# Kernel tuning notes

Measured on AMD Instinct MI355X. Metric: run time of the kernel, lower is better.

Reference implementation:

```python
import jax, jax.numpy as jnp
from jax import lax
import numpy as np

K = 2000      # self.k: entries kept per sample
T_SC = 3      # number of IHT iterations
DN = ('NCHW', 'OIHW', 'NCHW')


def keep_k_largest(X, k):
    # Per-sample hard threshold: keep the k largest-magnitude entries of the
    # flattened [C,H,W] activations, zero the rest (exactly k kept, as in argsort).
    B = X.shape[0]
    flat = X.reshape(B, -1)                                # [B, N]
    _, idx = lax.top_k(jnp.abs(flat), k)                   # [B, k]
    vals = jnp.take_along_axis(flat, idx, axis=1)          # [B, k]
    out = jnp.zeros_like(flat).at[jnp.arange(B)[:, None], idx].set(vals)
    return out.reshape(X.shape)


def _D_apply(X, W_D):
    # ConvTranspose2d(numb_atom -> dp_channels), stride 1, no padding:
    # full correlation with the spatially flipped, io-swapped kernel.
    kh, kw = W_D.shape[2], W_D.shape[3]
    Wt = jnp.flip(jnp.transpose(W_D, (1, 0, 2, 3)), (2, 3))  # [dp, atoms, kh, kw]
    return lax.conv_general_dilated(X, Wt, (1, 1),
                                    [(kh - 1, kh - 1), (kw - 1, kw - 1)],
                                    dimension_numbers=DN)


def _Dt_apply(Z, W_D):
    # Conv2d(dp_channels -> numb_atom) VALID; D_trans.weight = D.weight.permute(0,1,3,2)
    Wt = jnp.transpose(W_D, (0, 1, 3, 2))                  # [atoms, dp, kh, kw]
    return lax.conv_general_dilated(Z, Wt, (1, 1), 'VALID', dimension_numbers=DN)


def setup_inputs() -> dict:
    key = jax.random.key(0)
    k1, k2, k3 = jax.random.split(key, 3)
    Y = jax.random.normal(k1, (32, 3, 64, 64), jnp.float32)
    X0 = jax.random.normal(k2, (32, 128, 57, 57), jnp.float32)   # random init X in forward
    W_D = jax.random.normal(k3, (128, 3, 8, 8), jnp.float32) * 0.05
    return {"Y": Y, "X0": X0, "W_D": W_D}


def reference(Y, X0, W_D):
    # HT_arg = X - D_trans(D(X) - Y); then T_SC hard-threshold iterations.
    HT_arg = X0 - _Dt_apply(_D_apply(X0, W_D) - Y, W_D)
    X = HT_arg
    for i in range(T_SC):
        X = keep_k_largest(HT_arg, K)
        if i < T_SC - 1:  # final HT_arg update in the original is unused
            HT_arg = X - _Dt_apply(_D_apply(X, W_D) - Y, W_D)
    return X
```

## Files before the change

### kernel.cpp

```cpp
#include <hip/hip_runtime.h>

#define BATCH 32
#define ATOMS 128
#define CCH 3
#define XH 57
#define XW 57
#define OHH 64
#define OWW 64
#define KSEL 2000
#define PIX (XH*XW)
#define NPS (ATOMS*PIX)
#define NTOT (BATCH*NPS)
#define RPS (CCH*OHH*OWW)
#define RTOT (BATCH*RPS)
#define CANDCAP 32768
#define NW 24576
#define NWC 32768
#define ZWORDS (32*2048*2 + 32)

__global__ __launch_bounds__(256) void prep_k(const float* __restrict__ Wg,
    double* __restrict__ WDd, float* __restrict__ Wt2f,
    float* __restrict__ Wcand, const float* __restrict__ Y,
    double* __restrict__ Rd, unsigned* __restrict__ zbuf) {
  int e = blockIdx.x * 256 + threadIdx.x;
  if (e < NW) {
    {
      int kw = e & 7; int t = e >> 3; int c = t % 3; t /= 3; int kh = t & 7; int a = t >> 3;
      WDd[e] = (double)Wg[(a*3 + c)*64 + kh*8 + kw];
    }
    {
      int a = e & 127; int t = e >> 7; int j = t & 7; int i = (t >> 3) & 7; int c = t >> 6;
      Wt2f[e] = Wg[(a*3 + c)*64 + j*8 + i];
    }
  }
  if (e < NWC) {
    int a = e >> 8, r = e & 255;
    float v = 0.0f;
    if (r < 192) {
      int c = r >> 6, ii = (r >> 3) & 7, jj = r & 7;
      v = Wg[(a*3 + c)*64 + jj*8 + ii];
    }
    Wcand[e] = v;
  }
  if (e < RTOT) Rd[e] = -(double)Y[e];
  if (e < ZWORDS) zbuf[e] = 0;
}

__global__ __launch_bounds__(256) void convD_k(const float* __restrict__ X,
    const double* __restrict__ WDd, double* __restrict__ Rd) {
  __shared__ double Xs[4][11][72];
  int p = blockIdx.x;
  int lg = (p & 7) * 256 + (p >> 3);
  int b = lg >> 6; int rem = lg & 63;
  int band = rem >> 2, quarter = rem & 3;
  int row0 = band * 4;
  int a_base = quarter * 32;
  int tid = threadIdx.x;
  int ox = tid & 63;
  int wv = __builtin_amdgcn_readfirstlane(tid >> 6);
  const float* Xb = X + (size_t)b * NPS;

  double acc[4][3];
#pragma unroll
  for (int ty = 0; ty < 4; ++ty)
#pragma unroll
    for (int c = 0; c < 3; ++c) acc[ty][c] = 0.0;

  for (int ch = 0; ch < 8; ++ch) {
    __syncthreads();
    for (int e = tid; e < 4 * 11 * 72; e += 256) {
      int ai = e / 792; int rem2 = e - ai * 792;
      int r = rem2 / 72; int ss = rem2 - r * 72;
      int gy = row0 - 7 + r;
      int xcol = ss - 7;
      int a = a_base + ch * 4 + ai;
      float v = 0.0f;
      if ((unsigned)xcol < (unsigned)XW && (unsigned)gy < (unsigned)XH)
        v = Xb[a * PIX + gy * XW + xcol];
      Xs[ai][r][ss] = (double)v;
    }
    __syncthreads();
    {
      int a = a_base + ch * 4 + wv;
      const double* Wa = WDd + a * 192;
#pragma unroll
      for (int r = 0; r < 11; ++r) {
        int gy = row0 - 7 + r;
        if ((unsigned)gy >= (unsigned)XH) continue;
        double xd[8];
#pragma unroll
        for (int t = 0; t < 8; ++t) xd[t] = Xs[wv][r][ox + t];
#pragma unroll
        for (int ty = 0; ty < 4; ++ty) {
          int kh = ty + 7 - r;
          if ((unsigned)kh < 8u) {
            const double* Wk = Wa + kh * 24;
#pragma unroll
            for (int kw = 0; kw < 8; ++kw) {
              acc[ty][0] = fma(xd[7 - kw], Wk[kw],      acc[ty][0]);
              acc[ty][1] = fma(xd[7 - kw], Wk[8 + kw],  acc[ty][1]);
              acc[ty][2] = fma(xd[7 - kw], Wk[16 + kw], acc[ty][2]);
            }
          }
        }
      }
    }
  }
#pragma unroll
  for (int ty = 0; ty < 4; ++ty) {
    int oy = row0 + ty;
#pragma unroll
    for (int c = 0; c < 3; ++c)
      atomicAdd(&Rd[((size_t)(b * CCH + c) << 12) + (oy << 6) + ox], acc[ty][c]);
  }
}

__global__ __launch_bounds__(256) void convD_sparse_k(const float* __restrict__ Wg,
    const int* __restrict__ nzidx, const float* __restrict__ nzval,
    const float* __restrict__ Y, float* __restrict__ R) {
  __shared__ double accd[512];
  __shared__ float Wf[8192];
  __shared__ int   li[KSEL];
  __shared__ float lv[KSEL];
  int p = blockIdx.x;
  int lg = (p & 7) * 96 + (p >> 3);
  int s = lg / 24; int r = lg % 24; int c = r >> 3; int band = r & 7;
  int row0 = band * 8;
  int tid = threadIdx.x;
  for (int e = tid; e < 512; e += 256) accd[e] = 0.0;
  for (int e = tid; e < 8192; e += 256) {
    int a = e >> 6, k2 = e & 63;
    Wf[e] = Wg[(a * 3 + c) * 64 + k2];
  }
  for (int e = tid; e < KSEL; e += 256) {
    li[e] = nzidx[s * KSEL + e];
    lv[e] = nzval[s * KSEL + e];
  }
  __syncthreads();
  int slot = tid >> 3, kw = tid & 7;
  for (int e = slot; e < KSEL; e += 32) {
    int idx = li[e];
    int a = (int)((unsigned)idx / 3249u);
    int pp = idx - a * 3249;
    int y = (int)((unsigned)pp / 57u);
    int x = pp - y * 57;
    int dy = y - row0;
    if (dy < -7 || dy > 7) continue;
    double val = (double)lv[e];
    const float* wp = Wf + (a << 6) + kw;
#pragma unroll
    for (int kh = 0; kh < 8; ++kh) {
      int rr = dy + kh;
      if ((unsigned)rr < 8u)
        __hip_atomic_fetch_add(&accd[(rr << 6) + x + kw],
                               val * (double)wp[kh << 3],
                               __ATOMIC_RELAXED, __HIP_MEMORY_SCOPE_WORKGROUP);
    }
  }
  __syncthreads();
  const float* Yb = Y + (((size_t)(s * CCH + c)) << 12) + (row0 << 6);
  float* Rb = R + (((size_t)(s * CCH + c)) << 12) + (row0 << 6);
  for (int e = tid; e < 512; e += 256)
    Rb[e] = (float)(accd[e] - (double)Yb[e]);
}

template <typename TR>
__global__ __launch_bounds__(256) void convDt_k(const TR* __restrict__ R,
    const float* __restrict__ Wt2f, const float* __restrict__ Xprev,
    float* __restrict__ HT, unsigned* __restrict__ g1) {
  __shared__ float Rl[3][15][72];
  __shared__ unsigned hh[1024];
  int p = blockIdx.x;
  int lg = (p & 7) * 512 + (p >> 3);
  int b = lg >> 7; int rem = lg & 127; int ag = rem >> 3; int by = rem & 7;
  int row0 = by * 8;
  int a0 = ag * 8;
  int tid = threadIdx.x;
  for (int e = tid; e < 1024; e += 256) hh[e] = 0;
  for (int e = tid; e < 3 * 15 * 72; e += 256) {
    int c = e / (15 * 72); int r2 = e - c * (15 * 72);
    int rr = r2 / 72; int cc = r2 - rr * 72;
    int gr = row0 + rr;
    float v = 0.0f;
    if (cc < OWW && gr < OHH)
      v = (float)R[((size_t)(b * CCH + c) << 12) + (gr << 6) + cc];
    Rl[c][rr][cc] = v;
  }
  __syncthreads();
  int x = tid & 63, yg = tid >> 6;
  int yb = yg * 2;
  float acc[8][2];
#pragma unroll
  for (int aa = 0; aa < 8; ++aa) { acc[aa][0] = 0.0f; acc[aa][1] = 0.0f; }

#pragma unroll 1
  for (int c = 0; c < 3; ++c) {
#pragma unroll 1
    for (int j = 0; j < 8; ++j) {
      float rw[9];
#pragma unroll
      for (int r = 0; r < 9; ++r) rw[r] = Rl[c][yb + r][x + j];
#pragma unroll
      for (int i = 0; i < 8; ++i) {
        const float* wp = Wt2f + ((c * 8 + i) * 8 + j) * 128 + a0;
#pragma unroll
        for (int aa = 0; aa < 8; ++aa) {
          float w = wp[aa];
          acc[aa][0] = fmaf(rw[i + 0], w, acc[aa][0]);
          acc[aa][1] = fmaf(rw[i + 1], w, acc[aa][1]);
        }
      }
    }
  }
  if (x < XW) {
#pragma unroll
    for (int ty = 0; ty < 2; ++ty) {
      int yy = row0 + yb + ty;
      if (yy < XH) {
#pragma unroll
        for (int aa = 0; aa < 8; ++aa) {
          size_t xo = (size_t)(b * ATOMS + a0 + aa) * PIX + yy * XW + x;
          float fv = Xprev[xo] - acc[aa][ty];
          HT[xo] = fv;
          unsigned u = __float_as_uint(fv) & 0x7fffffffu;
          unsigned bin = u >> 20;
          atomicAdd(&hh[bin >> 1], 1u << ((bin & 1) << 4));
        }
      }
    }
  }
  __syncthreads();
  unsigned* gp = g1 + (size_t)b * 2048;
  for (int e = tid; e < 1024; e += 256) {
    unsigned v = hh[e];
    unsigned lo = v & 0xffffu, hi = v >> 16;
    if (lo) atomicAdd(&gp[2 * e], lo);
    if (hi) atomicAdd(&gp[2 * e + 1], hi);
  }
}

__global__ __launch_bounds__(256) void histwrite_k(const float* __restrict__ HT,
    const unsigned* __restrict__ g1, int* __restrict__ cand,
    int* __restrict__ candcnt, float* __restrict__ candprev,
    float* Xo, const float* prevX) {
  __shared__ unsigned part[256];
  __shared__ int lidx[4096];
  __shared__ float lprev[4096];
  __shared__ int lcnt, lbase, b1_sh;
  int tid = threadIdx.x;
  int s = blockIdx.x >> 5;
  int chunk = blockIdx.x & 31;
  const unsigned* hg1 = g1 + (size_t)s * 2048;
  unsigned psum = 0;
#pragma unroll
  for (int e = 0; e < 8; ++e) psum += hg1[tid * 8 + e];
  part[tid] = psum;
  if (tid == 0) lcnt = 0;
  __syncthreads();
  if (tid == 0) {
    int Kv = KSEL;
    unsigned cumBefore = 0;
    int bsel = 0;
    for (int q = 255; q >= 0; --q) {
      unsigned ps = part[q];
      if ((int)(cumBefore + ps) >= Kv) {
        for (int e = q * 8 + 7;; --e) {
          unsigned c2 = cumBefore + hg1[e];
          if ((int)c2 >= Kv) { bsel = e; break; }
          cumBefore = c2;
        }
        break;
      }
      cumBefore += ps;
    }
    b1_sh = bsel;
  }
  __syncthreads();
  unsigned blo = (unsigned)(b1_sh > 0 ? b1_sh - 1 : 0);
  size_t sbase = (size_t)s * NPS;
  const uint4* U4 = (const uint4*)(HT + sbase);
  const float4* P4 = (const float4*)(prevX + sbase);
  float4* X4 = (float4*)(Xo + sbase);
  for (int i4 = chunk * 256 + tid; i4 < NPS / 4; i4 += 32 * 256) {
    uint4 v = U4[i4];
    float4 pv = P4[i4];
    unsigned uu[4] = {v.x, v.y, v.z, v.w};
    float pp[4] = {pv.x, pv.y, pv.z, pv.w};
    float oo[4];
#pragma unroll
    for (int t = 0; t < 4; ++t) {
      int il = i4 * 4 + t;
      unsigned u = uu[t] & 0x7fffffffu;
      unsigned bin = u >> 20;
      if (bin >= blo) {
        oo[t] = __uint_as_float(uu[t]);
        int pos = atomicAdd(&lcnt, 1);
        if (pos < 4096) { lidx[pos] = il; lprev[pos] = pp[t]; }
      } else {
        oo[t] = 0.0f;
      }
    }
    X4[i4] = make_float4(oo[0], oo[1], oo[2], oo[3]);
  }
  __syncthreads();
  if (tid == 0) {
    int n = lcnt < 4096 ? lcnt : 4096;
    lbase = atomicAdd(&candcnt[s], n);
  }
  __syncthreads();
  int n = lcnt < 4096 ? lcnt : 4096;
  for (int e = tid; e < n; e += 256) {
    int g = lbase + e;
    if (g < CANDCAP) {
      cand[s * CANDCAP + g] = lidx[e];
      candprev[s * CANDCAP + g] = lprev[e];
    }
  }
}

template <typename TR>
__global__ __launch_bounds__(256) void recompute_k(const TR* __restrict__ R,
    const float* __restrict__ Wcand, const int* __restrict__ cand,
    const int* __restrict__ candcnt, const float* __restrict__ candprev,
    float* __restrict__ candval, unsigned* __restrict__ g1x) {
  __shared__ unsigned hx[2048];
  int s = blockIdx.x >> 5;
  int chunk = blockIdx.x & 31;
  int tid = threadIdx.x;
  for (int e = tid; e < 2048; e += 256) hx[e] = 0;
  __syncthreads();
  int n = candcnt[s];
  if (n > CANDCAP) n = CANDCAP;
  const TR* Rb = R + ((size_t)(s * 3) << 12);
  for (int e = chunk * 256 + tid; e < n; e += 32 * 256) {
    int i = cand[s * CANDCAP + e];
    int a = (int)((unsigned)i / 3249u);
    int p = i - a * 3249;
    int y = (int)((unsigned)p / 57u);
    int x = p - y * 57;
    double xprev = (double)candprev[s * CANDCAP + e];
    const float* wa = Wcand + (a << 8);
    double acc = 0.0;
    for (int c = 0; c < 3; ++c) {
#pragma unroll
      for (int ii = 0; ii < 8; ++ii) {
        const TR* rrow = Rb + (c << 12) + ((y + ii) << 6) + x;
        const float* wrow = wa + (c * 8 + ii) * 8;
#pragma unroll
        for (int jj = 0; jj < 8; ++jj)
          acc = fma((double)rrow[jj], (double)wrow[jj], acc);
      }
    }
    float cf = (float)(xprev - acc);
    candval[s * CANDCAP + e] = cf;
    unsigned u = __float_as_uint(cf) & 0x7fffffffu;
    atomicAdd(&hx[u >> 20], 1u);
  }
  __syncthreads();
  unsigned* gp = g1x + (size_t)s * 2048;
  for (int e = tid; e < 2048; e += 256)
    if (hx[e]) atomicAdd(&gp[e], hx[e]);
}

__global__ __launch_bounds__(256) void pass3_k(const int* __restrict__ cand,
    int* __restrict__ candcnt, const float* __restrict__ candval,
    unsigned* __restrict__ g1, unsigned* __restrict__ g1x,
    float* __restrict__ Xo, int* __restrict__ nzidx, float* __restrict__ nzval,
    int emit) {
  int s = blockIdx.x;
  __shared__ unsigned h[1024];
  __shared__ unsigned part[256];
  __shared__ int eqidx[1024];
  __shared__ int kidx[2048];
  __shared__ float kval[2048];
  __shared__ int eqn, kcnt;
  __shared__ unsigned tau_sh;
  __shared__ int k3_sh, cutoff_sh, b1_sh, k1_sh, b2_sh, k2_sh;
  int t = threadIdx.x;
  unsigned* hx = g1x + (size_t)s * 2048;
  unsigned s1 = 0;
#pragma unroll
  for (int e = 0; e < 8; ++e) s1 += hx[t * 8 + e];
  part[t] = s1;
  for (int e = t; e < 1024; e += 256) h[e] = 0;
  if (t == 0) { eqn = 0; kcnt = 0; }
  __syncthreads();
  if (t == 0) {
    int Kv = KSEL;
    unsigned cumBefore = 0;
    int bsel = 0;
    for (int q = 255; q >= 0; --q) {
      unsigned ps = part[q];
      if ((int)(cumBefore + ps) >= Kv) {
        for (int e = q * 8 + 7;; --e) {
          unsigned c2 = cumBefore + hx[e];
          if ((int)c2 >= Kv) { bsel = e; break; }
          cumBefore = c2;
        }
        break;
      }
      cumBefore += ps;
    }
    b1_sh = bsel;
    k1_sh = KSEL - (int)cumBefore;
  }
  __syncthreads();
  int n = candcnt[s];
  if (n > CANDCAP) n = CANDCAP;
  const int* cs = cand + s * CANDCAP;
  const float* cv = candval + s * CANDCAP;
  unsigned b1x = (unsigned)b1_sh;
  for (int e = t; e < n; e += 256) {
    unsigned u = __float_as_uint(cv[e]) & 0x7fffffffu;
    if ((u >> 20) == b1x) atomicAdd(&h[(u >> 10) & 1023], 1u);
  }
  __syncthreads();
  part[t] = h[t * 4] + h[t * 4 + 1] + h[t * 4 + 2] + h[t * 4 + 3];
  __syncthreads();
  if (t == 0) {
    int Kv = k1_sh;
    unsigned cumBefore = 0;
    int bsel = 0;
    for (int q = 255; q >= 0; --q) {
      unsigned ps = part[q];
      if ((int)(cumBefore + ps) >= Kv) {
        for (int e = q * 4 + 3;; --e) {
          unsigned c2 = cumBefore + h[e];
          if ((int)c2 >= Kv) { bsel = e; break; }
          cumBefore = c2;
        }
        break;
      }
      cumBefore += ps;
    }
    b2_sh = bsel;
    k2_sh = Kv - (int)cumBefore;
  }
  __syncthreads();
  for (int e = t; e < 1024; e += 256) h[e] = 0;
  __syncthreads();
  unsigned pre21 = (b1x << 10) | (unsigned)b2_sh;
  for (int e = t; e < n; e += 256) {
    unsigned u = __float_as_uint(cv[e]) & 0x7fffffffu;
    if ((u >> 10) == pre21) atomicAdd(&h[u & 1023], 1u);
  }
  __syncthreads();
  if (t == 0) {
    int Kv = k2_sh;
    unsigned cumBefore = 0;
    int b3 = 0;
    for (int e = 1023; e >= 0; --e) {
      unsigned c2 = cumBefore + h[e];
      if ((int)c2 >= Kv) { b3 = e; break; }
      cumBefore = c2;
    }
    tau_sh = (pre21 << 10) | (unsigned)b3;
    k3_sh = Kv - (int)cumBefore;
  }
  __syncthreads();
  unsigned tau = tau_sh;
  for (int e = t; e < n; e += 256) {
    unsigned u = __float_as_uint(cv[e]) & 0x7fffffffu;
    if (u == tau) {
      int pos = atomicAdd(&eqn, 1);
      if (pos < 1024) eqidx[pos] = cs[e];
    }
  }
  __syncthreads();
  if (t == 0) {
    int m = eqn < 1024 ? eqn : 1024;
    int k3 = k3_sh;
    int cutoff;
    if (k3 >= m) {
      cutoff = 0x7fffffff;
    } else {
      int last = -1;
      for (int r = 0; r < k3; ++r) {
        int mn = 0x7fffffff;
        for (int q = 0; q < m; ++q) {
          int v = eqidx[q];
          if (v > last && v < mn) mn = v;
        }
        last = mn;
      }
      cutoff = last;
    }
    cutoff_sh = cutoff;
  }
  __syncthreads();
  int co = cutoff_sh;
  float* Xs = Xo + (size_t)s * NPS;
  for (int e = t; e < n; e += 256) {
    int i = cs[e];
    float cf = cv[e];
    unsigned u = __float_as_uint(cf) & 0x7fffffffu;
    bool keep = (u > tau) || (u == tau && i <= co);
    Xs[i] = keep ? cf : 0.0f;
    if (keep && emit) {
      int pos = atomicAdd(&kcnt, 1);
      if (pos < 2048) { kidx[pos] = i; kval[pos] = cf; }
    }
  }
  __syncthreads();
  if (emit) {
    int kn = kcnt < KSEL ? kcnt : KSEL;
    for (int e = t; e < kn; e += 256) {
      nzidx[s * KSEL + e] = kidx[e];
      nzval[s * KSEL + e] = kval[e];
    }
  }
  unsigned* hg1 = g1 + (size_t)s * 2048;
  for (int e = t; e < 2048; e += 256) { hg1[e] = 0; hx[e] = 0; }
  if (t == 0) candcnt[s] = 0;
}

extern "C" void kernel_launch(void* const* d_in, const int* in_sizes, int n_in,
                              void* d_out, int out_size, void* d_ws, size_t ws_size,
                              hipStream_t stream) {
  const float* Y  = (const float*)d_in[0];
  const float* X0 = (const float*)d_in[1];
  const float* Wg = (const float*)d_in[2];
  float* Xout = (float*)d_out;

  double* WDd  = (double*)d_ws;
  float* Wt2f  = (float*)(WDd + NW);
  float* Wcand = Wt2f + NW;
  float* HT   = Wcand + NWC;
  float* Rbuf = HT + NTOT;
  double* Rd  = (double*)(Rbuf + RTOT);
  unsigned* g1 = (unsigned*)(Rd + RTOT);
  unsigned* g1x = g1 + 32 * 2048;
  int* candcnt = (int*)(g1x + 32 * 2048);
  int* cand = candcnt + 32;
  float* candval = (float*)(cand + 32 * CANDCAP);
  float* candprev = candval + 32 * CANDCAP;
  int* nzidx = (int*)(candprev + 32 * CANDCAP);
  float* nzval = (float*)(nzidx + 32 * KSEL);

  prep_k<<<dim3((RTOT + 255) / 256), dim3(256), 0, stream>>>(
      Wg, WDd, Wt2f, Wcand, Y, Rd, g1);

  for (int it = 0; it < 3; ++it) {
    if (it == 0) {
      convD_k<<<dim3(2048), dim3(256), 0, stream>>>(X0, WDd, Rd);
      convDt_k<double><<<dim3(4096), dim3(256), 0, stream>>>(Rd, Wt2f, X0, HT, g1);
    } else {
      convD_sparse_k<<<dim3(BATCH * CCH * 8), dim3(256), 0, stream>>>(
          Wg, nzidx, nzval, Y, Rbuf);
      convDt_k<float><<<dim3(4096), dim3(256), 0, stream>>>(Rbuf, Wt2f,
          (const float*)Xout, HT, g1);
    }
    histwrite_k<<<dim3(BATCH * 32), dim3(256), 0, stream>>>(
        HT, g1, cand, candcnt, candprev, Xout, (it == 0) ? X0 : (const float*)Xout);
    if (it == 0) {
      recompute_k<double><<<dim3(BATCH * 32), dim3(256), 0, stream>>>(
          Rd, Wcand, cand, candcnt, candprev, candval, g1x);
    } else {
      recompute_k<float><<<dim3(BATCH * 32), dim3(256), 0, stream>>>(
          Rbuf, Wcand, cand, candcnt, candprev, candval, g1x);
    }
    int emit = (it < 2) ? 1 : 0;
    pass3_k<<<dim3(BATCH), dim3(256), 0, stream>>>(
        cand, candcnt, candval, g1, g1x, Xout, nzidx, nzval, emit);
  }
}
```

Measured before the change: 955.2 us.

## Fuse candidate recompute into histwrite and build refine histogram in pass3

Merges the separate recompute kernel into histwrite, so candidates are recomputed in double precision right after selection. The previous X is read in place instead of being staged through candprev, and Xout is written only where elements are not candidates. The coarse histogram of the recomputed values is now built inside pass3, which drops the g1x global buffer and its atomics. This removes one launch per iteration and the full prevX read stream. The cost is pass3 doing an extra pass over candidates with only 32 blocks, and a candidate margin widened by one extra bin.

```diff
diff --git a/kernel.cpp b/kernel.cpp
--- a/kernel.cpp
+++ b/kernel.cpp
@@ -16,7 +16,8 @@
 #define CANDCAP 32768
 #define NW 24576
 #define NWC 32768
-#define ZWORDS (32*2048*2 + 32)
+#define LCAP 6144
+#define ZWORDS (32*2048 + 32)
 
 __global__ __launch_bounds__(256) void prep_k(const float* __restrict__ Wg,
     double* __restrict__ WDd, float* __restrict__ Wt2f,
@@ -239,13 +240,14 @@
   }
 }
 
+template <typename TR>
 __global__ __launch_bounds__(256) void histwrite_k(const float* __restrict__ HT,
-    const unsigned* __restrict__ g1, int* __restrict__ cand,
-    int* __restrict__ candcnt, float* __restrict__ candprev,
-    float* Xo, const float* prevX) {
+    const unsigned* __restrict__ g1, const TR* __restrict__ R,
+    const float* __restrict__ Wcand, const float* Xp,
+    int* __restrict__ cand, int* __restrict__ candcnt,
+    float* __restrict__ candval, float* Xo) {
   __shared__ unsigned part[256];
-  __shared__ int lidx[4096];
-  __shared__ float lprev[4096];
+  __shared__ int lidx[LCAP];
   __shared__ int lcnt, lbase, b1_sh;
   int tid = threadIdx.x;
   int s = blockIdx.x >> 5;
@@ -276,69 +278,47 @@
     b1_sh = bsel;
   }
   __syncthreads();
-  unsigned blo = (unsigned)(b1_sh > 0 ? b1_sh - 1 : 0);
+  unsigned blo = (unsigned)(b1_sh >= 2 ? b1_sh - 2 : 0);
   size_t sbase = (size_t)s * NPS;
   const uint4* U4 = (const uint4*)(HT + sbase);
-  const float4* P4 = (const float4*)(prevX + sbase);
   float4* X4 = (float4*)(Xo + sbase);
   for (int i4 = chunk * 256 + tid; i4 < NPS / 4; i4 += 32 * 256) {
     uint4 v = U4[i4];
-    float4 pv = P4[i4];
     unsigned uu[4] = {v.x, v.y, v.z, v.w};
-    float pp[4] = {pv.x, pv.y, pv.z, pv.w};
-    float oo[4];
+    int m = 0;
 #pragma unroll
     for (int t = 0; t < 4; ++t) {
-      int il = i4 * 4 + t;
       unsigned u = uu[t] & 0x7fffffffu;
-      unsigned bin = u >> 20;
-      if (bin >= blo) {
-        oo[t] = __uint_as_float(uu[t]);
+      if ((u >> 20) >= blo) {
+        m |= 1 << t;
         int pos = atomicAdd(&lcnt, 1);
-        if (pos < 4096) { lidx[pos] = il; lprev[pos] = pp[t]; }
-      } else {
-        oo[t] = 0.0f;
-      }
-    }
-    X4[i4] = make_float4(oo[0], oo[1], oo[2], oo[3]);
+        if (pos < LCAP) lidx[pos] = i4 * 4 + t;
+      }
+    }
+    if (m == 0) {
+      X4[i4] = make_float4(0.0f, 0.0f, 0.0f, 0.0f);
+    } else {
+#pragma unroll
+      for (int t = 0; t < 4; ++t)
+        if (!(m & (1 << t))) Xo[sbase + i4 * 4 + t] = 0.0f;
+    }
   }
   __syncthreads();
   if (tid == 0) {
-    int n = lcnt < 4096 ? lcnt : 4096;
-    lbase = atomicAdd(&candcnt[s], n);
-  }
-  __syncthreads();
-  int n = lcnt < 4096 ? lcnt : 4096;
-  for (int e = tid; e < n; e += 256) {
+    int nn = lcnt < LCAP ? lcnt : LCAP;
+    lbase = atomicAdd(&candcnt[s], nn);
+  }
+  __syncthreads();
+  int nn = lcnt < LCAP ? lcnt : LCAP;
+  const TR* Rb = R + ((size_t)(s * 3) << 12);
+  for (int e = tid; e < nn; e += 256) {
+    int i = lidx[e];
     int g = lbase + e;
-    if (g < CANDCAP) {
-      cand[s * CANDCAP + g] = lidx[e];
-      candprev[s * CANDCAP + g] = lprev[e];
-    }
-  }
-}
-
-template <typename TR>
-__global__ __launch_bounds__(256) void recompute_k(const TR* __restrict__ R,
-    const float* __restrict__ Wcand, const int* __restrict__ cand,
-    const int* __restrict__ candcnt, const float* __restrict__ candprev,
-    float* __restrict__ candval, unsigned* __restrict__ g1x) {
-  __shared__ unsigned hx[2048];
-  int s = blockIdx.x >> 5;
-  int chunk = blockIdx.x & 31;
-  int tid = threadIdx.x;
-  for (int e = tid; e < 2048; e += 256) hx[e] = 0;
-  __syncthreads();
-  int n = candcnt[s];
-  if (n > CANDCAP) n = CANDCAP;
-  const TR* Rb = R + ((size_t)(s * 3) << 12);
-  for (int e = chunk * 256 + tid; e < n; e += 32 * 256) {
-    int i = cand[s * CANDCAP + e];
     int a = (int)((unsigned)i / 3249u);
     int p = i - a * 3249;
     int y = (int)((unsigned)p / 57u);
     int x = p - y * 57;
-    double xprev = (double)candprev[s * CANDCAP + e];
+    double xprev = (double)Xp[sbase + i];
     const float* wa = Wcand + (a << 8);
     double acc = 0.0;
     for (int c = 0; c < 3; ++c) {
@@ -352,23 +332,19 @@
       }
     }
     float cf = (float)(xprev - acc);
-    candval[s * CANDCAP + e] = cf;
-    unsigned u = __float_as_uint(cf) & 0x7fffffffu;
-    atomicAdd(&hx[u >> 20], 1u);
-  }
-  __syncthreads();
-  unsigned* gp = g1x + (size_t)s * 2048;
-  for (int e = tid; e < 2048; e += 256)
-    if (hx[e]) atomicAdd(&gp[e], hx[e]);
+    if (g < CANDCAP) {
+      cand[s * CANDCAP + g] = i;
+      candval[s * CANDCAP + g] = cf;
+    }
+  }
 }
 
 __global__ __launch_bounds__(256) void pass3_k(const int* __restrict__ cand,
     int* __restrict__ candcnt, const float* __restrict__ candval,
-    unsigned* __restrict__ g1, unsigned* __restrict__ g1x,
-    float* __restrict__ Xo, int* __restrict__ nzidx, float* __restrict__ nzval,
-    int emit) {
+    unsigned* __restrict__ g1, float* __restrict__ Xo,
+    int* __restrict__ nzidx, float* __restrict__ nzval, int emit) {
   int s = blockIdx.x;
-  __shared__ unsigned h[1024];
+  __shared__ unsigned h[2048];
   __shared__ unsigned part[256];
   __shared__ int eqidx[1024];
   __shared__ int kidx[2048];
@@ -377,13 +353,22 @@
   __shared__ unsigned tau_sh;
   __shared__ int k3_sh, cutoff_sh, b1_sh, k1_sh, b2_sh, k2_sh;
   int t = threadIdx.x;
-  unsigned* hx = g1x + (size_t)s * 2048;
+  int n = candcnt[s];
+  if (n > CANDCAP) n = CANDCAP;
+  const int* cs = cand + s * CANDCAP;
+  const float* cv = candval + s * CANDCAP;
+  for (int e = t; e < 2048; e += 256) h[e] = 0;
+  if (t == 0) { eqn = 0; kcnt = 0; }
+  __syncthreads();
+  for (int e = t; e < n; e += 256) {
+    unsigned u = __float_as_uint(cv[e]) & 0x7fffffffu;
+    atomicAdd(&h[u >> 20], 1u);
+  }
+  __syncthreads();
   unsigned s1 = 0;
 #pragma unroll
-  for (int e = 0; e < 8; ++e) s1 += hx[t * 8 + e];
+  for (int e = 0; e < 8; ++e) s1 += h[t * 8 + e];
   part[t] = s1;
-  for (int e = t; e < 1024; e += 256) h[e] = 0;
-  if (t == 0) { eqn = 0; kcnt = 0; }
   __syncthreads();
   if (t == 0) {
     int Kv = KSEL;
@@ -393,7 +378,7 @@
       unsigned ps = part[q];
       if ((int)(cumBefore + ps) >= Kv) {
         for (int e = q * 8 + 7;; --e) {
-          unsigned c2 = cumBefore + hx[e];
+          unsigned c2 = cumBefore + h[e];
           if ((int)c2 >= Kv) { bsel = e; break; }
           cumBefore = c2;
         }
@@ -405,11 +390,9 @@
     k1_sh = KSEL - (int)cumBefore;
   }
   __syncthreads();
-  int n = candcnt[s];
-  if (n > CANDCAP) n = CANDCAP;
-  const int* cs = cand + s * CANDCAP;
-  const float* cv = candval + s * CANDCAP;
   unsigned b1x = (unsigned)b1_sh;
+  for (int e = t; e < 1024; e += 256) h[e] = 0;
+  __syncthreads();
   for (int e = t; e < n; e += 256) {
     unsigned u = __float_as_uint(cv[e]) & 0x7fffffffu;
     if ((u >> 20) == b1x) atomicAdd(&h[(u >> 10) & 1023], 1u);
@@ -510,7 +493,7 @@
     }
   }
   unsigned* hg1 = g1 + (size_t)s * 2048;
-  for (int e = t; e < 2048; e += 256) { hg1[e] = 0; hx[e] = 0; }
+  for (int e = t; e < 2048; e += 256) hg1[e] = 0;
   if (t == 0) candcnt[s] = 0;
 }
 
@@ -529,12 +512,10 @@
   float* Rbuf = HT + NTOT;
   double* Rd  = (double*)(Rbuf + RTOT);
   unsigned* g1 = (unsigned*)(Rd + RTOT);
-  unsigned* g1x = g1 + 32 * 2048;
-  int* candcnt = (int*)(g1x + 32 * 2048);
+  int* candcnt = (int*)(g1 + 32 * 2048);
   int* cand = candcnt + 32;
   float* candval = (float*)(cand + 32 * CANDCAP);
-  float* candprev = candval + 32 * CANDCAP;
-  int* nzidx = (int*)(candprev + 32 * CANDCAP);
+  int* nzidx = (int*)(candval + 32 * CANDCAP);
   float* nzval = (float*)(nzidx + 32 * KSEL);
 
   prep_k<<<dim3((RTOT + 255) / 256), dim3(256), 0, stream>>>(
@@ -544,23 +525,18 @@
     if (it == 0) {
       convD_k<<<dim3(2048), dim3(256), 0, stream>>>(X0, WDd, Rd);
       convDt_k<double><<<dim3(4096), dim3(256), 0, stream>>>(Rd, Wt2f, X0, HT, g1);
+      histwrite_k<double><<<dim3(BATCH * 32), dim3(256), 0, stream>>>(
+          HT, g1, Rd, Wcand, X0, cand, candcnt, candval, Xout);
     } else {
       convD_sparse_k<<<dim3(BATCH * CCH * 8), dim3(256), 0, stream>>>(
           Wg, nzidx, nzval, Y, Rbuf);
       convDt_k<float><<<dim3(4096), dim3(256), 0, stream>>>(Rbuf, Wt2f,
           (const float*)Xout, HT, g1);
-    }
-    histwrite_k<<<dim3(BATCH * 32), dim3(256), 0, stream>>>(
-        HT, g1, cand, candcnt, candprev, Xout, (it == 0) ? X0 : (const float*)Xout);
-    if (it == 0) {
-      recompute_k<double><<<dim3(BATCH * 32), dim3(256), 0, stream>>>(
-          Rd, Wcand, cand, candcnt, candprev, candval, g1x);
-    } else {
-      recompute_k<float><<<dim3(BATCH * 32), dim3(256), 0, stream>>>(
-          Rbuf, Wcand, cand, candcnt, candprev, candval, g1x);
+      histwrite_k<float><<<dim3(BATCH * 32), dim3(256), 0, stream>>>(
+          HT, g1, Rbuf, Wcand, (const float*)Xout, cand, candcnt, candval, Xout);
     }
     int emit = (it < 2) ? 1 : 0;
     pass3_k<<<dim3(BATCH), dim3(256), 0, stream>>>(
-        cand, candcnt, candval, g1, g1x, Xout, nzidx, nzval, emit);
-  }
-}
+        cand, candcnt, candval, g1, Xout, nzidx, nzval, emit);
+  }
+}
```

Result: no change. 942.4 us (-1.3%).
